# Kernel optimization log

Hardware: AMD Instinct MI355X
Metric: run time of the kernel (lower is better)

## Reference

```python
import jax, jax.numpy as jnp
import numpy as np

N = 768      # n_proto (number of class prototypes)
D = 128      # trans_feat_num
H = D // 16  # edge-MLP hidden = 8
A = 312      # semantic attribute dim
INIT_TEMP = 0.1
VTEMP = 10.0
STEMP = 10.0
EPS = 1e-8


def _layer_norm(x, g, b, eps=1e-5):
    m = x.mean(-1, keepdims=True)
    v = ((x - m) ** 2).mean(-1, keepdims=True)
    return (x - m) / jnp.sqrt(v + eps) * g + b


def _instance_norm_rows(x, eps=1e-5):
    # torch InstanceNorm1d on 2D input: unbatched (C, L) -> normalize each row, no affine
    m = x.mean(-1, keepdims=True)
    v = ((x - m) ** 2).mean(-1, keepdims=True)
    return (x - m) / jnp.sqrt(v + eps)


def _init_edge(x, temp):
    # pairwise cosine similarity + row softmax
    nrm = jnp.linalg.norm(x, axis=1)
    sim = (x @ x.T) / jnp.maximum(nrm[:, None] * nrm[None, :], EPS)
    return jax.nn.softmax(sim / temp, axis=-1)


def _edge_update(proto, last_edge, W1, b1, W2, b2, temp):
    n, d = proto.shape
    # O(n^2) pairwise squared differences  -> [n*n, d]
    feat = ((proto[:, None, :] - proto[None, :, :]) ** 2).reshape(n * n, d)
    h = jax.nn.relu(_instance_norm_rows(feat @ W1.T + b1))  # [n*n, H]
    e = jnp.tanh(h @ W2.T + b2).reshape(n, n)
    return jax.nn.softmax(e * (last_edge + EPS) / temp, axis=-1)


def _node_update(proto, last_edge, edge, W, b, g, beta):
    extra = last_edge @ proto          # cross-modal message (dist_injection)
    p = edge @ proto                   # same-modal aggregation
    return jax.nn.relu(_layer_norm((p + extra) @ W.T + b, g, beta)) + p


def setup_inputs() -> dict:
    key = jax.random.key(0)
    ks = jax.random.split(key, 9)
    rn = lambda k, shape, s=1.0: jax.random.normal(k, shape, dtype=jnp.float32) * s
    return {
        "visual_proto": rn(ks[0], (N, D)),
        "semantic_proto": rn(ks[1], (N, D)),
        "attribute": rn(ks[2], (N, A)),
        "Wvn": rn(ks[3], (D, D), 0.08), "bvn": jnp.zeros((D,), jnp.float32),
        "gvn": jnp.ones((D,), jnp.float32), "betavn": jnp.zeros((D,), jnp.float32),
        "Wve1": rn(ks[4], (H, D), 0.1), "bve1": jnp.zeros((H,), jnp.float32),
        "Wve2": rn(ks[5], (1, H), 0.3), "bve2": jnp.zeros((1,), jnp.float32),
        "Wsn": rn(ks[6], (D, D), 0.08), "bsn": jnp.zeros((D,), jnp.float32),
        "gsn": jnp.ones((D,), jnp.float32), "betasn": jnp.zeros((D,), jnp.float32),
        "Wse1": rn(ks[7], (H, D), 0.1), "bse1": jnp.zeros((H,), jnp.float32),
        "Wse2": rn(ks[8], (1, H), 0.3), "bse2": jnp.zeros((1,), jnp.float32),
    }


def reference(visual_proto, semantic_proto, attribute,
              Wvn, bvn, gvn, betavn, Wve1, bve1, Wve2, bve2,
              Wsn, bsn, gsn, betasn, Wse1, bse1, Wse2, bse2):
    ve = _init_edge(visual_proto, INIT_TEMP)
    se = _init_edge(attribute, INIT_TEMP)
    vp = _node_update(visual_proto, se, ve, Wvn, bvn, gvn, betavn)
    ve2 = _edge_update(vp, ve, Wve1, bve1, Wve2, bve2, VTEMP)
    sp = _node_update(semantic_proto, ve2, se, Wsn, bsn, gsn, betasn)
    se2 = _edge_update(sp, se, Wse1, bse1, Wse2, bse2, STEMP)
    return vp, sp, ve2, se2
```

## Files before the change

kernel.cpp:

```cpp
#include <hip/hip_runtime.h>
#include <math.h>

#define NN 768
#define DD 128
#define AA 312
#define HH 8
#define CEPS 1e-8f

typedef __attribute__((ext_vector_type(2))) float v2f;

__device__ __forceinline__ v2f vfma2(v2f a, v2f b, v2f c) {
#if __has_builtin(__builtin_elementwise_fma)
    return __builtin_elementwise_fma(a, b, c);
#else
    v2f r;
    r.x = fmaf(a.x, b.x, c.x);
    r.y = fmaf(a.y, b.y, c.y);
    return r;
#endif
}

__device__ __forceinline__ float wave_sum(float v) {
    #pragma unroll
    for (int o = 32; o; o >>= 1) v += __shfl_down(v, o, 64);
    return v;
}
__device__ __forceinline__ float wave_max(float v) {
    #pragma unroll
    for (int o = 32; o; o >>= 1) v = fmaxf(v, __shfl_down(v, o, 64));
    return v;
}

template <int COLS>
__device__ void gram_tile(const float* __restrict__ A, float invtemp, float* __restrict__ sim,
                          int i0, int j0, int tid, float* As, float* Bs) {
    const int tx = tid & 15, ty = tid >> 4;
    const int lr = tid >> 3, lc4 = (tid & 7) * 4;
    float acc00 = 0.f, acc01 = 0.f, acc10 = 0.f, acc11 = 0.f;
    float si0 = 0.f, si1 = 0.f, sj0 = 0.f, sj1 = 0.f;
    for (int kc = 0; kc < COLS; kc += 32) {
        float4 av, bv;
        if (kc + lc4 + 4 <= COLS) {
            av = *(const float4*)(A + (size_t)(i0 + lr) * COLS + kc + lc4);
            bv = *(const float4*)(A + (size_t)(j0 + lr) * COLS + kc + lc4);
        } else {
            float ta[4], tb[4];
            #pragma unroll
            for (int l = 0; l < 4; ++l) {
                int c = kc + lc4 + l;
                ta[l] = (c < COLS) ? A[(size_t)(i0 + lr) * COLS + c] : 0.f;
                tb[l] = (c < COLS) ? A[(size_t)(j0 + lr) * COLS + c] : 0.f;
            }
            av = make_float4(ta[0], ta[1], ta[2], ta[3]);
            bv = make_float4(tb[0], tb[1], tb[2], tb[3]);
        }
        __syncthreads();
        As[(lc4 + 0) * 34 + lr] = av.x; As[(lc4 + 1) * 34 + lr] = av.y;
        As[(lc4 + 2) * 34 + lr] = av.z; As[(lc4 + 3) * 34 + lr] = av.w;
        Bs[(lc4 + 0) * 34 + lr] = bv.x; Bs[(lc4 + 1) * 34 + lr] = bv.y;
        Bs[(lc4 + 2) * 34 + lr] = bv.z; Bs[(lc4 + 3) * 34 + lr] = bv.w;
        __syncthreads();
        #pragma unroll
        for (int k = 0; k < 32; ++k) {
            float2 aa = *(const float2*)&As[k * 34 + 2 * ty];
            float2 bb = *(const float2*)&Bs[k * 34 + 2 * tx];
            acc00 = fmaf(aa.x, bb.x, acc00);
            acc01 = fmaf(aa.x, bb.y, acc01);
            acc10 = fmaf(aa.y, bb.x, acc10);
            acc11 = fmaf(aa.y, bb.y, acc11);
            si0 = fmaf(aa.x, aa.x, si0);
            si1 = fmaf(aa.y, aa.y, si1);
            sj0 = fmaf(bb.x, bb.x, sj0);
            sj1 = fmaf(bb.y, bb.y, sj1);
        }
    }
    const float ni0 = sqrtf(si0), ni1 = sqrtf(si1);
    const float nj0 = sqrtf(sj0), nj1 = sqrtf(sj1);
    float* s0 = sim + (size_t)(i0 + 2 * ty) * NN + j0 + 2 * tx;
    float* s1 = s0 + NN;
    s0[0] = acc00 / fmaxf(ni0 * nj0, CEPS) * invtemp;
    s0[1] = acc01 / fmaxf(ni0 * nj1, CEPS) * invtemp;
    s1[0] = acc10 / fmaxf(ni1 * nj0, CEPS) * invtemp;
    s1[1] = acc11 / fmaxf(ni1 * nj1, CEPS) * invtemp;
}

__global__ __launch_bounds__(256) void gram_prep_kernel(
    const float* __restrict__ visual, const float* __restrict__ attribute,
    const float* __restrict__ Wvn, const float* __restrict__ Wsn, float* __restrict__ simv,
    float* __restrict__ sima, float* __restrict__ WvnT, float* __restrict__ WsnT) {
    __shared__ __align__(16) float smem[2176];
    const int tid = threadIdx.x;
    const int task = blockIdx.x;
    if (task < 576) {
        gram_tile<DD>(visual, 10.f, simv, (task / 24) * 32, (task % 24) * 32, tid, smem,
                      smem + 1088);
    } else if (task < 1152) {
        const int rem = task - 576;
        gram_tile<AA>(attribute, 10.f, sima, (rem / 24) * 32, (rem % 24) * 32, tid, smem,
                      smem + 1088);
    } else {
        const int u = task - 1152;
        const float* S = (u >= 16) ? Wsn : Wvn;
        float* Dt = (u >= 16) ? WsnT : WvnT;
        const int tile = u & 15;
        const int c0 = (tile & 3) * 32, r0 = (tile >> 2) * 32;
        const int tx = tid & 31, ty = tid >> 5;
        #pragma unroll
        for (int rr = ty; rr < 32; rr += 8)
            smem[rr * 33 + tx] = S[(size_t)(r0 + rr) * DD + c0 + tx];
        __syncthreads();
        #pragma unroll
        for (int rr = ty; rr < 32; rr += 8)
            Dt[(size_t)(c0 + rr) * DD + r0 + tx] = smem[tx * 33 + rr];
    }
}

__device__ void block_softmax768(float* buf, int tid, float* red) {
    const int w = tid >> 6, lane = tid & 63;
    float v0 = buf[tid];
    float v1 = (tid < NN - 512) ? buf[tid + 512] : -3.4e38f;
    float m = wave_max(fmaxf(v0, v1));
    if (lane == 0) red[w] = m;
    __syncthreads();
    m = red[0];
    #pragma unroll
    for (int i = 1; i < 8; ++i) m = fmaxf(m, red[i]);
    float e0 = __expf(v0 - m);
    float e1 = (tid < NN - 512) ? __expf(v1 - m) : 0.f;
    float sw = wave_sum(e0 + e1);
    if (lane == 0) red[8 + w] = sw;
    __syncthreads();
    float s = 0.f;
    #pragma unroll
    for (int i = 0; i < 8; ++i) s += red[8 + i];
    const float inv = 1.f / s;
    buf[tid] = e0 * inv;
    if (tid < NN - 512) buf[tid + 512] = e1 * inv;
    __syncthreads();
}

__device__ void softmax_row_to(const float* __restrict__ vr, float* __restrict__ dst, int tid,
                               float* red) {
    float v0 = vr[tid], v1 = vr[tid + 256], v2 = vr[tid + 512];
    float m = wave_max(fmaxf(fmaxf(v0, v1), v2));
    if ((tid & 63) == 0) red[tid >> 6] = m;
    __syncthreads();
    m = fmaxf(fmaxf(red[0], red[1]), fmaxf(red[2], red[3]));
    float e0 = __expf(v0 - m), e1 = __expf(v1 - m), e2 = __expf(v2 - m);
    float sw = wave_sum(e0 + e1 + e2);
    if ((tid & 63) == 0) red[4 + (tid >> 6)] = sw;
    __syncthreads();
    const float s = red[4] + red[5] + red[6] + red[7];
    const float inv = 1.f / s;
    dst[tid] = e0 * inv;
    dst[tid + 256] = e1 * inv;
    dst[tid + 512] = e2 * inv;
    __syncthreads();
}

__global__ __launch_bounds__(512) void node1_kernel(
    const float* __restrict__ P, const float* __restrict__ srcEp,
    const float* __restrict__ srcEx, const float* __restrict__ WT, const float* __restrict__ b,
    const float* __restrict__ g, const float* __restrict__ beta, float* __restrict__ out,
    float* __restrict__ outT) {
    __shared__ __align__(16) float ep[2][NN], ex[2][NN];
    __shared__ __align__(16) float pp[4][2][DD], xx[4][2][DD];
    __shared__ __align__(16) float qs[2][DD], tps[2][2][DD];
    __shared__ float red[16];
    const int i0 = blockIdx.x * 2;
    const int tid = threadIdx.x;
    const int s = (tid >> 7) & 3, d = tid & 127;
    #pragma unroll
    for (int r = 0; r < 2; ++r)
        for (int k = tid; k < NN; k += 512) {
            ep[r][k] = srcEp[(size_t)(i0 + r) * NN + k];
            ex[r][k] = srcEx[(size_t)(i0 + r) * NN + k];
        }
    __syncthreads();
    block_softmax768(ep[0], tid, red);
    block_softmax768(ep[1], tid, red);
    block_softmax768(ex[0], tid, red);
    block_softmax768(ex[1], tid, red);
    v2f P0 = {0.f, 0.f}, X0 = {0.f, 0.f}, P1 = {0.f, 0.f}, X1 = {0.f, 0.f};
    const int kb = s * 192;
    #pragma unroll 4
    for (int kk = 0; kk < 192; kk += 2) {
        const int k = kb + kk;
        const float a0 = P[(size_t)k * DD + d];
        const float a1 = P[(size_t)(k + 1) * DD + d];
        v2f pv; pv.x = a0; pv.y = a1;
        const v2f e0v = *(const v2f*)&ep[0][k];
        const v2f x0v = *(const v2f*)&ex[0][k];
        const v2f e1v = *(const v2f*)&ep[1][k];
        const v2f x1v = *(const v2f*)&ex[1][k];
        P0 = vfma2(e0v, pv, P0);
        X0 = vfma2(x0v, pv, X0);
        P1 = vfma2(e1v, pv, P1);
        X1 = vfma2(x1v, pv, X1);
    }
    pp[s][0][d] = P0.x + P0.y; xx[s][0][d] = X0.x + X0.y;
    pp[s][1][d] = P1.x + P1.y; xx[s][1][d] = X1.x + X1.y;
    __syncthreads();
    const int rr = (tid >> 7) & 1;
    float preg = 0.f;
    if (tid < 256) {
        float p = pp[0][rr][d] + pp[1][rr][d] + pp[2][rr][d] + pp[3][rr][d];
        float x = xx[0][rr][d] + xx[1][rr][d] + xx[2][rr][d] + xx[3][rr][d];
        qs[rr][d] = p + x;
        preg = p;
    }
    __syncthreads();
    {
        const int sc = tid >> 8, rr2 = (tid >> 7) & 1;
        v2f acc; acc.x = (sc == 0) ? b[d] : 0.f; acc.y = 0.f;
        const int c0 = sc * 64;
        #pragma unroll 4
        for (int c = c0; c < c0 + 64; c += 2) {
            v2f wv; wv.x = WT[(size_t)c * DD + d]; wv.y = WT[(size_t)(c + 1) * DD + d];
            const v2f qq = *(const v2f*)&qs[rr2][c];
            acc = vfma2(qq, wv, acc);
        }
        tps[sc][rr2][d] = acc.x + acc.y;
    }
    __syncthreads();
    float tval = 0.f;
    if (tid < 256) tval = tps[0][rr][d] + tps[1][rr][d];
    float sm = wave_sum(tid < 256 ? tval : 0.f);
    if ((tid & 63) == 0) red[tid >> 6] = sm;
    __syncthreads();
    if (tid < 256) tval -= (red[2 * rr] + red[2 * rr + 1]) * (1.f / DD);
    float s2 = wave_sum(tid < 256 ? tval * tval : 0.f);
    if ((tid & 63) == 0) red[8 + (tid >> 6)] = s2;
    __syncthreads();
    if (tid < 256) {
        const float var = (red[8 + 2 * rr] + red[8 + 2 * rr + 1]) * (1.f / DD);
        const float ln = tval * rsqrtf(var + 1e-5f) * g[d] + beta[d];
        const float val = fmaxf(ln, 0.f) + preg;
        out[(size_t)(i0 + rr) * DD + d] = val;
        outT[(size_t)d * NN + i0 + rr] = val;
    }
}

__device__ __forceinline__ float edge_mlp_tail(float* z, const float* __restrict__ b1,
                                               const float* __restrict__ W2, float b2s) {
    float mean = 0.f;
    #pragma unroll
    for (int r = 0; r < HH; ++r) { z[r] += b1[r]; mean += z[r]; }
    mean *= (1.f / HH);
    float var = 0.f;
    #pragma unroll
    for (int r = 0; r < HH; ++r) { float dv = z[r] - mean; var += dv * dv; }
    var *= (1.f / HH);
    const float istd = rsqrtf(var + 1e-5f);
    float acc = b2s;
    #pragma unroll
    for (int r = 0; r < HH; ++r) {
        float hn = fmaxf((z[r] - mean) * istd, 0.f);
        acc = fmaf(hn, W2[r], acc);
    }
    return tanhf(acc);
}

template <bool FUSE>
__global__ __launch_bounds__(256) void edge_fused_kernel(
    const float* __restrict__ PR, const float* __restrict__ PRt,
    const float* __restrict__ lastSim, const float* __restrict__ W1,
    const float* __restrict__ b1, const float* __restrict__ W2, const float* __restrict__ b2,
    float invtemp, float* __restrict__ E2,
    const float* __restrict__ simaRows, const float* __restrict__ S,
    const float* __restrict__ WT, const float* __restrict__ nb, const float* __restrict__ ng,
    const float* __restrict__ nbeta, float* __restrict__ outN, float* __restrict__ outNT) {
    const int i = blockIdx.x;
    const int tid = threadIdx.x;
    __shared__ __align__(16) float pi[DD];
    __shared__ __align__(16) float4 w_s[HH][DD / 4];
    __shared__ __align__(16) float lrow[NN];
    __shared__ __align__(16) float aux[NN];
    __shared__ __align__(16) float ve2row[NN];
    __shared__ __align__(16) float part[4][DD];
    __shared__ __align__(16) float qvv[DD];
    __shared__ float red[16];
    if (tid < DD) pi[tid] = PR[(size_t)i * DD + tid];
    ((float4*)w_s)[tid] = ((const float4*)W1)[tid];
    softmax_row_to(lastSim + (size_t)i * NN, lrow, tid, red);
    if (FUSE) softmax_row_to(simaRows + (size_t)i * NN, aux, tid, red);
    const int j0 = tid, j1 = tid + 256, j2 = tid + 512;
    v2f z0[HH], z1[HH], z2[HH];
    #pragma unroll
    for (int r = 0; r < HH; ++r) {
        z0[r] = (v2f){0.f, 0.f}; z1[r] = (v2f){0.f, 0.f}; z2[r] = (v2f){0.f, 0.f};
    }
    const float4* p4 = (const float4*)pi;
    for (int k4 = 0; k4 < DD / 4; ++k4) {
        const float4 pv4 = p4[k4];
        v2f pa; pa.x = pv4.x; pa.y = pv4.y;
        v2f pb; pb.x = pv4.z; pb.y = pv4.w;
        const float* r0 = PRt + (size_t)(k4 * 4) * NN;
        const float* r1 = r0 + NN;
        const float* r2 = r1 + NN;
        const float* r3 = r2 + NN;
        v2f ja0, jb0, ja1, jb1, ja2, jb2;
        ja0.x = r0[j0]; ja0.y = r1[j0]; jb0.x = r2[j0]; jb0.y = r3[j0];
        ja1.x = r0[j1]; ja1.y = r1[j1]; jb1.x = r2[j1]; jb1.y = r3[j1];
        ja2.x = r0[j2]; ja2.y = r1[j2]; jb2.x = r2[j2]; jb2.y = r3[j2];
        v2f da0 = pa - ja0, db0 = pb - jb0;
        v2f da1 = pa - ja1, db1 = pb - jb1;
        v2f da2 = pa - ja2, db2 = pb - jb2;
        v2f sa0 = da0 * da0, sb0 = db0 * db0;
        v2f sa1 = da1 * da1, sb1 = db1 * db1;
        v2f sa2 = da2 * da2, sb2 = db2 * db2;
        #pragma unroll
        for (int r = 0; r < HH; ++r) {
            const float4 w = w_s[r][k4];
            v2f wa; wa.x = w.x; wa.y = w.y;
            v2f wb; wb.x = w.z; wb.y = w.w;
            z0[r] = vfma2(wa, sa0, z0[r]); z0[r] = vfma2(wb, sb0, z0[r]);
            z1[r] = vfma2(wa, sa1, z1[r]); z1[r] = vfma2(wb, sb1, z1[r]);
            z2[r] = vfma2(wa, sa2, z2[r]); z2[r] = vfma2(wb, sb2, z2[r]);
        }
    }
    float za[HH], zb[HH], zc[HH];
    #pragma unroll
    for (int r = 0; r < HH; ++r) {
        za[r] = z0[r].x + z0[r].y;
        zb[r] = z1[r].x + z1[r].y;
        zc[r] = z2[r].x + z2[r].y;
    }
    const float b2s = b2[0];
    float v0 = edge_mlp_tail(za, b1, W2, b2s) * (lrow[j0] + CEPS) * invtemp;
    float v1 = edge_mlp_tail(zb, b1, W2, b2s) * (lrow[j1] + CEPS) * invtemp;
    float v2 = edge_mlp_tail(zc, b1, W2, b2s) * (lrow[j2] + CEPS) * invtemp;
    float m = wave_max(fmaxf(fmaxf(v0, v1), v2));
    if ((tid & 63) == 0) red[tid >> 6] = m;
    __syncthreads();
    m = fmaxf(fmaxf(red[0], red[1]), fmaxf(red[2], red[3]));
    float e0 = __expf(v0 - m), e1 = __expf(v1 - m), e2 = __expf(v2 - m);
    float sw = wave_sum(e0 + e1 + e2);
    if ((tid & 63) == 0) red[4 + (tid >> 6)] = sw;
    __syncthreads();
    const float ssum = red[4] + red[5] + red[6] + red[7];
    const float inv = 1.f / ssum;
    float* Er = E2 + (size_t)i * NN;
    const float o0 = e0 * inv, o1 = e1 * inv, o2 = e2 * inv;
    Er[j0] = o0; Er[j1] = o1; Er[j2] = o2;
    if (FUSE) {
        ve2row[j0] = o0; ve2row[j1] = o1; ve2row[j2] = o2;
        __syncthreads();
        const int d = tid & 127, h = tid >> 7;
        v2f accp = {0.f, 0.f}, accx = {0.f, 0.f};
        const int k0 = h * 384;
        #pragma unroll 4
        for (int kk = 0; kk < 384; kk += 2) {
            const int k = k0 + kk;
            v2f sv; sv.x = S[(size_t)k * DD + d]; sv.y = S[(size_t)(k + 1) * DD + d];
            const v2f sev = *(const v2f*)&aux[k];
            const v2f vev = *(const v2f*)&ve2row[k];
            accp = vfma2(sev, sv, accp);
            accx = vfma2(vev, sv, accx);
        }
        part[h][d] = accp.x + accp.y;
        part[2 + h][d] = accx.x + accx.y;
        __syncthreads();
        float preg = 0.f;
        if (tid < DD) {
            preg = part[0][d] + part[1][d];
            const float x = part[2][d] + part[3][d];
            qvv[d] = preg + x;
        }
        __syncthreads();
        {
            v2f acc; acc.x = (h == 0) ? nb[d] : 0.f; acc.y = 0.f;
            const int c0 = h * 64;
            #pragma unroll 4
            for (int c = c0; c < c0 + 64; c += 2) {
                v2f wv; wv.x = WT[(size_t)c * DD + d]; wv.y = WT[(size_t)(c + 1) * DD + d];
                const v2f qq = *(const v2f*)&qvv[c];
                acc = vfma2(qq, wv, acc);
            }
            __syncthreads();
            part[h][d] = acc.x + acc.y;
        }
        __syncthreads();
        float tval = 0.f;
        if (tid < DD) {
            tval = part[0][d] + part[1][d];
            float sm2 = wave_sum(tval);
            if ((tid & 63) == 0) red[tid >> 6] = sm2;
        }
        __syncthreads();
        if (tid < DD) {
            const float mean = (red[0] + red[1]) * (1.f / DD);
            const float dv = tval - mean;
            float s2 = wave_sum(dv * dv);
            if ((tid & 63) == 0) red[4 + (tid >> 6)] = s2;
        }
        __syncthreads();
        if (tid < DD) {
            const float mean = (red[0] + red[1]) * (1.f / DD);
            const float var = (red[4] + red[5]) * (1.f / DD);
            const float ln = (tval - mean) * rsqrtf(var + 1e-5f) * ng[d] + nbeta[d];
            const float val = fmaxf(ln, 0.f) + preg;
            outN[(size_t)i * DD + d] = val;
            outNT[(size_t)d * NN + i] = val;
        }
    }
}

extern "C" void kernel_launch(void* const* d_in, const int* in_sizes, int n_in, void* d_out,
                              int out_size, void* d_ws, size_t ws_size, hipStream_t stream) {
    const float* visual    = (const float*)d_in[0];
    const float* semantic  = (const float*)d_in[1];
    const float* attribute = (const float*)d_in[2];
    const float* Wvn  = (const float*)d_in[3];
    const float* bvn  = (const float*)d_in[4];
    const float* gvn  = (const float*)d_in[5];
    const float* betavn = (const float*)d_in[6];
    const float* Wve1 = (const float*)d_in[7];
    const float* bve1 = (const float*)d_in[8];
    const float* Wve2 = (const float*)d_in[9];
    const float* bve2 = (const float*)d_in[10];
    const float* Wsn  = (const float*)d_in[11];
    const float* bsn  = (const float*)d_in[12];
    const float* gsn  = (const float*)d_in[13];
    const float* betasn = (const float*)d_in[14];
    const float* Wse1 = (const float*)d_in[15];
    const float* bse1 = (const float*)d_in[16];
    const float* Wse2 = (const float*)d_in[17];
    const float* bse2 = (const float*)d_in[18];

    float* out = (float*)d_out;
    float* vp  = out;
    float* sp  = out + 98304;
    float* ve2 = out + 196608;
    float* se2 = out + 786432;

    float* ws   = (float*)d_ws;
    float* simv = ws;
    float* sima = ws + 589824;
    float* vpT  = ws + 1179648;
    float* spT  = ws + 1277952;
    float* WvnT = ws + 1376256;
    float* WsnT = ws + 1392640;

    gram_prep_kernel<<<1184, 256, 0, stream>>>(visual, attribute, Wvn, Wsn, simv, sima, WvnT,
                                               WsnT);
    node1_kernel<<<NN / 2, 512, 0, stream>>>(visual, simv, sima, WvnT, bvn, gvn, betavn, vp,
                                             vpT);
    edge_fused_kernel<true><<<NN, 256, 0, stream>>>(vp, vpT, simv, Wve1, bve1, Wve2, bve2,
                                                    0.1f, ve2, sima, semantic, WsnT, bsn, gsn,
                                                    betasn, sp, spT);
    edge_fused_kernel<false><<<NN, 256, 0, stream>>>(sp, spT, sima, Wse1, bse1, Wse2, bse2,
                                                     0.1f, se2, sima, semantic, WsnT, bsn, gsn,
                                                     betasn, nullptr, nullptr);
}
```

Measured before the change: 197.3 us.

## Use 384-thread edge blocks with two columns per thread and packed gram FMAs

The edge kernels now launch 384 threads per row instead of 256. Each thread handles two adjacent columns, so the transposed prototype rows can be read with float2 loads, and the softmax, reductions and aggregation splits are reworked for six waves. The gram tile inner loop is also rewritten to use packed two-wide FMAs. The aim is more parallelism per row, fewer registers per thread and vectorised memory access, at the cost of more threads idling in the 128-wide node-update stages.

```diff
diff --git a/kernel.cpp b/kernel.cpp
--- a/kernel.cpp
+++ b/kernel.cpp
@@ -36,8 +36,8 @@
                           int i0, int j0, int tid, float* As, float* Bs) {
     const int tx = tid & 15, ty = tid >> 4;
     const int lr = tid >> 3, lc4 = (tid & 7) * 4;
-    float acc00 = 0.f, acc01 = 0.f, acc10 = 0.f, acc11 = 0.f;
-    float si0 = 0.f, si1 = 0.f, sj0 = 0.f, sj1 = 0.f;
+    v2f acc0 = {0.f, 0.f}, acc1 = {0.f, 0.f};
+    v2f si = {0.f, 0.f}, sj = {0.f, 0.f};
     for (int kc = 0; kc < COLS; kc += 32) {
         float4 av, bv;
         if (kc + lc4 + 4 <= COLS) {
@@ -62,26 +62,24 @@
         __syncthreads();
         #pragma unroll
         for (int k = 0; k < 32; ++k) {
-            float2 aa = *(const float2*)&As[k * 34 + 2 * ty];
-            float2 bb = *(const float2*)&Bs[k * 34 + 2 * tx];
-            acc00 = fmaf(aa.x, bb.x, acc00);
-            acc01 = fmaf(aa.x, bb.y, acc01);
-            acc10 = fmaf(aa.y, bb.x, acc10);
-            acc11 = fmaf(aa.y, bb.y, acc11);
-            si0 = fmaf(aa.x, aa.x, si0);
-            si1 = fmaf(aa.y, aa.y, si1);
-            sj0 = fmaf(bb.x, bb.x, sj0);
-            sj1 = fmaf(bb.y, bb.y, sj1);
-        }
-    }
-    const float ni0 = sqrtf(si0), ni1 = sqrtf(si1);
-    const float nj0 = sqrtf(sj0), nj1 = sqrtf(sj1);
+            const v2f a = *(const v2f*)&As[k * 34 + 2 * ty];
+            const v2f b = *(const v2f*)&Bs[k * 34 + 2 * tx];
+            v2f ax; ax.x = a.x; ax.y = a.x;
+            v2f ay; ay.x = a.y; ay.y = a.y;
+            acc0 = vfma2(ax, b, acc0);
+            acc1 = vfma2(ay, b, acc1);
+            si = vfma2(a, a, si);
+            sj = vfma2(b, b, sj);
+        }
+    }
+    const float ni0 = sqrtf(si.x), ni1 = sqrtf(si.y);
+    const float nj0 = sqrtf(sj.x), nj1 = sqrtf(sj.y);
     float* s0 = sim + (size_t)(i0 + 2 * ty) * NN + j0 + 2 * tx;
     float* s1 = s0 + NN;
-    s0[0] = acc00 / fmaxf(ni0 * nj0, CEPS) * invtemp;
-    s0[1] = acc01 / fmaxf(ni0 * nj1, CEPS) * invtemp;
-    s1[0] = acc10 / fmaxf(ni1 * nj0, CEPS) * invtemp;
-    s1[1] = acc11 / fmaxf(ni1 * nj1, CEPS) * invtemp;
+    s0[0] = acc0.x / fmaxf(ni0 * nj0, CEPS) * invtemp;
+    s0[1] = acc0.y / fmaxf(ni0 * nj1, CEPS) * invtemp;
+    s1[0] = acc1.x / fmaxf(ni1 * nj0, CEPS) * invtemp;
+    s1[1] = acc1.y / fmaxf(ni1 * nj1, CEPS) * invtemp;
 }
 
 __global__ __launch_bounds__(256) void gram_prep_kernel(
@@ -139,22 +137,25 @@
     __syncthreads();
 }
 
-__device__ void softmax_row_to(const float* __restrict__ vr, float* __restrict__ dst, int tid,
-                               float* red) {
-    float v0 = vr[tid], v1 = vr[tid + 256], v2 = vr[tid + 512];
-    float m = wave_max(fmaxf(fmaxf(v0, v1), v2));
+__device__ void softmax_row_to384(const float* __restrict__ vr, float* __restrict__ dst,
+                                  int tid, float* red) {
+    float v0 = vr[tid], v1 = vr[tid + 384];
+    float m = wave_max(fmaxf(v0, v1));
     if ((tid & 63) == 0) red[tid >> 6] = m;
     __syncthreads();
-    m = fmaxf(fmaxf(red[0], red[1]), fmaxf(red[2], red[3]));
-    float e0 = __expf(v0 - m), e1 = __expf(v1 - m), e2 = __expf(v2 - m);
-    float sw = wave_sum(e0 + e1 + e2);
-    if ((tid & 63) == 0) red[4 + (tid >> 6)] = sw;
-    __syncthreads();
-    const float s = red[4] + red[5] + red[6] + red[7];
+    m = red[0];
+    #pragma unroll
+    for (int i = 1; i < 6; ++i) m = fmaxf(m, red[i]);
+    float e0 = __expf(v0 - m), e1 = __expf(v1 - m);
+    float sw = wave_sum(e0 + e1);
+    if ((tid & 63) == 0) red[8 + (tid >> 6)] = sw;
+    __syncthreads();
+    float s = 0.f;
+    #pragma unroll
+    for (int i = 0; i < 6; ++i) s += red[8 + i];
     const float inv = 1.f / s;
     dst[tid] = e0 * inv;
-    dst[tid + 256] = e1 * inv;
-    dst[tid + 512] = e2 * inv;
+    dst[tid + 384] = e1 * inv;
     __syncthreads();
 }
 
@@ -186,9 +187,7 @@
     #pragma unroll 4
     for (int kk = 0; kk < 192; kk += 2) {
         const int k = kb + kk;
-        const float a0 = P[(size_t)k * DD + d];
-        const float a1 = P[(size_t)(k + 1) * DD + d];
-        v2f pv; pv.x = a0; pv.y = a1;
+        v2f pv; pv.x = P[(size_t)k * DD + d]; pv.y = P[(size_t)(k + 1) * DD + d];
         const v2f e0v = *(const v2f*)&ep[0][k];
         const v2f x0v = *(const v2f*)&ex[0][k];
         const v2f e1v = *(const v2f*)&ep[1][k];
@@ -262,7 +261,7 @@
 }
 
 template <bool FUSE>
-__global__ __launch_bounds__(256) void edge_fused_kernel(
+__global__ __launch_bounds__(384) void edge_fused_kernel(
     const float* __restrict__ PR, const float* __restrict__ PRt,
     const float* __restrict__ lastSim, const float* __restrict__ W1,
     const float* __restrict__ b1, const float* __restrict__ W2, const float* __restrict__ b2,
@@ -277,80 +276,78 @@
     __shared__ __align__(16) float lrow[NN];
     __shared__ __align__(16) float aux[NN];
     __shared__ __align__(16) float ve2row[NN];
-    __shared__ __align__(16) float part[4][DD];
+    __shared__ __align__(16) float partp[3][DD], partx[3][DD];
     __shared__ __align__(16) float qvv[DD];
     __shared__ float red[16];
     if (tid < DD) pi[tid] = PR[(size_t)i * DD + tid];
-    ((float4*)w_s)[tid] = ((const float4*)W1)[tid];
-    softmax_row_to(lastSim + (size_t)i * NN, lrow, tid, red);
-    if (FUSE) softmax_row_to(simaRows + (size_t)i * NN, aux, tid, red);
-    const int j0 = tid, j1 = tid + 256, j2 = tid + 512;
-    v2f z0[HH], z1[HH], z2[HH];
-    #pragma unroll
-    for (int r = 0; r < HH; ++r) {
-        z0[r] = (v2f){0.f, 0.f}; z1[r] = (v2f){0.f, 0.f}; z2[r] = (v2f){0.f, 0.f};
-    }
+    if (tid < 256) ((float4*)w_s)[tid] = ((const float4*)W1)[tid];
+    softmax_row_to384(lastSim + (size_t)i * NN, lrow, tid, red);
+    if (FUSE) softmax_row_to384(simaRows + (size_t)i * NN, aux, tid, red);
+    const int j0 = tid * 2;
+    v2f zz0[HH], zz1[HH];
+    #pragma unroll
+    for (int r = 0; r < HH; ++r) { zz0[r] = (v2f){0.f, 0.f}; zz1[r] = (v2f){0.f, 0.f}; }
     const float4* p4 = (const float4*)pi;
+    #pragma unroll 2
     for (int k4 = 0; k4 < DD / 4; ++k4) {
         const float4 pv4 = p4[k4];
+        const float* r0 = PRt + (size_t)(k4 * 4) * NN;
+        const float2 f0 = *(const float2*)&r0[j0];
+        const float2 f1 = *(const float2*)&r0[NN + j0];
+        const float2 f2 = *(const float2*)&r0[2 * NN + j0];
+        const float2 f3 = *(const float2*)&r0[3 * NN + j0];
         v2f pa; pa.x = pv4.x; pa.y = pv4.y;
         v2f pb; pb.x = pv4.z; pb.y = pv4.w;
-        const float* r0 = PRt + (size_t)(k4 * 4) * NN;
-        const float* r1 = r0 + NN;
-        const float* r2 = r1 + NN;
-        const float* r3 = r2 + NN;
-        v2f ja0, jb0, ja1, jb1, ja2, jb2;
-        ja0.x = r0[j0]; ja0.y = r1[j0]; jb0.x = r2[j0]; jb0.y = r3[j0];
-        ja1.x = r0[j1]; ja1.y = r1[j1]; jb1.x = r2[j1]; jb1.y = r3[j1];
-        ja2.x = r0[j2]; ja2.y = r1[j2]; jb2.x = r2[j2]; jb2.y = r3[j2];
-        v2f da0 = pa - ja0, db0 = pb - jb0;
-        v2f da1 = pa - ja1, db1 = pb - jb1;
-        v2f da2 = pa - ja2, db2 = pb - jb2;
-        v2f sa0 = da0 * da0, sb0 = db0 * db0;
-        v2f sa1 = da1 * da1, sb1 = db1 * db1;
-        v2f sa2 = da2 * da2, sb2 = db2 * db2;
+        v2f ja0; ja0.x = f0.x; ja0.y = f1.x;
+        v2f jb0; jb0.x = f2.x; jb0.y = f3.x;
+        v2f ja1; ja1.x = f0.y; ja1.y = f1.y;
+        v2f jb1; jb1.x = f2.y; jb1.y = f3.y;
+        const v2f da0 = pa - ja0, db0 = pb - jb0;
+        const v2f da1 = pa - ja1, db1 = pb - jb1;
+        const v2f sa0 = da0 * da0, sb0 = db0 * db0;
+        const v2f sa1 = da1 * da1, sb1 = db1 * db1;
         #pragma unroll
         for (int r = 0; r < HH; ++r) {
             const float4 w = w_s[r][k4];
             v2f wa; wa.x = w.x; wa.y = w.y;
             v2f wb; wb.x = w.z; wb.y = w.w;
-            z0[r] = vfma2(wa, sa0, z0[r]); z0[r] = vfma2(wb, sb0, z0[r]);
-            z1[r] = vfma2(wa, sa1, z1[r]); z1[r] = vfma2(wb, sb1, z1[r]);
-            z2[r] = vfma2(wa, sa2, z2[r]); z2[r] = vfma2(wb, sb2, z2[r]);
-        }
-    }
-    float za[HH], zb[HH], zc[HH];
+            zz0[r] = vfma2(wa, sa0, zz0[r]); zz0[r] = vfma2(wb, sb0, zz0[r]);
+            zz1[r] = vfma2(wa, sa1, zz1[r]); zz1[r] = vfma2(wb, sb1, zz1[r]);
+        }
+    }
+    float za[HH], zb[HH];
     #pragma unroll
     for (int r = 0; r < HH; ++r) {
-        za[r] = z0[r].x + z0[r].y;
-        zb[r] = z1[r].x + z1[r].y;
-        zc[r] = z2[r].x + z2[r].y;
+        za[r] = zz0[r].x + zz0[r].y;
+        zb[r] = zz1[r].x + zz1[r].y;
     }
     const float b2s = b2[0];
     float v0 = edge_mlp_tail(za, b1, W2, b2s) * (lrow[j0] + CEPS) * invtemp;
-    float v1 = edge_mlp_tail(zb, b1, W2, b2s) * (lrow[j1] + CEPS) * invtemp;
-    float v2 = edge_mlp_tail(zc, b1, W2, b2s) * (lrow[j2] + CEPS) * invtemp;
-    float m = wave_max(fmaxf(fmaxf(v0, v1), v2));
+    float v1 = edge_mlp_tail(zb, b1, W2, b2s) * (lrow[j0 + 1] + CEPS) * invtemp;
+    float m = wave_max(fmaxf(v0, v1));
     if ((tid & 63) == 0) red[tid >> 6] = m;
     __syncthreads();
-    m = fmaxf(fmaxf(red[0], red[1]), fmaxf(red[2], red[3]));
-    float e0 = __expf(v0 - m), e1 = __expf(v1 - m), e2 = __expf(v2 - m);
-    float sw = wave_sum(e0 + e1 + e2);
-    if ((tid & 63) == 0) red[4 + (tid >> 6)] = sw;
-    __syncthreads();
-    const float ssum = red[4] + red[5] + red[6] + red[7];
+    m = red[0];
+    #pragma unroll
+    for (int k = 1; k < 6; ++k) m = fmaxf(m, red[k]);
+    float e0 = __expf(v0 - m), e1 = __expf(v1 - m);
+    float sw = wave_sum(e0 + e1);
+    if ((tid & 63) == 0) red[8 + (tid >> 6)] = sw;
+    __syncthreads();
+    float ssum = 0.f;
+    #pragma unroll
+    for (int k = 0; k < 6; ++k) ssum += red[8 + k];
     const float inv = 1.f / ssum;
-    float* Er = E2 + (size_t)i * NN;
-    const float o0 = e0 * inv, o1 = e1 * inv, o2 = e2 * inv;
-    Er[j0] = o0; Er[j1] = o1; Er[j2] = o2;
+    float2 ov; ov.x = e0 * inv; ov.y = e1 * inv;
+    *(float2*)&E2[(size_t)i * NN + j0] = ov;
     if (FUSE) {
-        ve2row[j0] = o0; ve2row[j1] = o1; ve2row[j2] = o2;
+        *(float2*)&ve2row[j0] = ov;
         __syncthreads();
         const int d = tid & 127, h = tid >> 7;
         v2f accp = {0.f, 0.f}, accx = {0.f, 0.f};
-        const int k0 = h * 384;
+        const int k0 = h * 256;
         #pragma unroll 4
-        for (int kk = 0; kk < 384; kk += 2) {
+        for (int kk = 0; kk < 256; kk += 2) {
             const int k = k0 + kk;
             v2f sv; sv.x = S[(size_t)k * DD + d]; sv.y = S[(size_t)(k + 1) * DD + d];
             const v2f sev = *(const v2f*)&aux[k];
@@ -358,32 +355,32 @@
             accp = vfma2(sev, sv, accp);
             accx = vfma2(vev, sv, accx);
         }
-        part[h][d] = accp.x + accp.y;
-        part[2 + h][d] = accx.x + accx.y;
+        partp[h][d] = accp.x + accp.y;
+        partx[h][d] = accx.x + accx.y;
         __syncthreads();
         float preg = 0.f;
         if (tid < DD) {
-            preg = part[0][d] + part[1][d];
-            const float x = part[2][d] + part[3][d];
+            preg = partp[0][d] + partp[1][d] + partp[2][d];
+            const float x = partx[0][d] + partx[1][d] + partx[2][d];
             qvv[d] = preg + x;
         }
         __syncthreads();
-        {
-            v2f acc; acc.x = (h == 0) ? nb[d] : 0.f; acc.y = 0.f;
-            const int c0 = h * 64;
+        if (tid < 256) {
+            const int hh = tid >> 7;
+            v2f acc; acc.x = (hh == 0) ? nb[d] : 0.f; acc.y = 0.f;
+            const int c0 = hh * 64;
             #pragma unroll 4
             for (int c = c0; c < c0 + 64; c += 2) {
                 v2f wv; wv.x = WT[(size_t)c * DD + d]; wv.y = WT[(size_t)(c + 1) * DD + d];
                 const v2f qq = *(const v2f*)&qvv[c];
                 acc = vfma2(qq, wv, acc);
             }
-            __syncthreads();
-            part[h][d] = acc.x + acc.y;
+            partx[hh][d] = acc.x + acc.y;
         }
         __syncthreads();
         float tval = 0.f;
         if (tid < DD) {
-            tval = part[0][d] + part[1][d];
+            tval = partx[0][d] + partx[1][d];
             float sm2 = wave_sum(tval);
             if ((tid & 63) == 0) red[tid >> 6] = sm2;
         }
@@ -392,12 +389,12 @@
             const float mean = (red[0] + red[1]) * (1.f / DD);
             const float dv = tval - mean;
             float s2 = wave_sum(dv * dv);
-            if ((tid & 63) == 0) red[4 + (tid >> 6)] = s2;
+            if ((tid & 63) == 0) red[8 + (tid >> 6)] = s2;
         }
         __syncthreads();
         if (tid < DD) {
             const float mean = (red[0] + red[1]) * (1.f / DD);
-            const float var = (red[4] + red[5]) * (1.f / DD);
+            const float var = (red[8] + red[9]) * (1.f / DD);
             const float ln = (tval - mean) * rsqrtf(var + 1e-5f) * ng[d] + nbeta[d];
             const float val = fmaxf(ln, 0.f) + preg;
             outN[(size_t)i * DD + d] = val;
@@ -446,10 +443,10 @@
                                                WsnT);
     node1_kernel<<<NN / 2, 512, 0, stream>>>(visual, simv, sima, WvnT, bvn, gvn, betavn, vp,
                                              vpT);
-    edge_fused_kernel<true><<<NN, 256, 0, stream>>>(vp, vpT, simv, Wve1, bve1, Wve2, bve2,
+    edge_fused_kernel<true><<<NN, 384, 0, stream>>>(vp, vpT, simv, Wve1, bve1, Wve2, bve2,
                                                     0.1f, ve2, sima, semantic, WsnT, bsn, gsn,
                                                     betasn, sp, spT);
-    edge_fused_kernel<false><<<NN, 256, 0, stream>>>(sp, spT, sima, Wse1, bse1, Wse2, bse2,
+    edge_fused_kernel<false><<<NN, 384, 0, stream>>>(sp, spT, sima, Wse1, bse1, Wse2, bse2,
                                                      0.1f, se2, sima, semantic, WsnT, bsn, gsn,
                                                      betasn, nullptr, nullptr);
 }
```

After: 218.4 us. 10.7% more time.
